# Kernel optimization log

Hardware: AMD Instinct MI355X
Metric: run time of the kernel (lower is better)

Reference implementation:

```python
import jax, jax.numpy as jnp
import numpy as np

NUM_GRAPHS = 128
EPS = 1e-5  # torch BatchNorm1d default eps


def setup_inputs() -> dict:
    key = jax.random.key(0)
    ks = jax.random.split(key, 24)
    N, E, NHE = 50000, 800000, 50000
    NODE_RAW, HEDGE_RAW, H, HH, HOUT = 92, 40, 128, 128, 256
    s = 0.05
    inp = {
        "x": jax.random.normal(ks[0], (N, NODE_RAW), jnp.float32),
        "hedge_attrs": jax.random.normal(ks[1], (NHE, HEDGE_RAW), jnp.float32),
        "inter_relations_index": jax.random.randint(ks[2], (3, E), 0, N, jnp.int64),
        "batch": jax.random.randint(ks[3], (N,), 0, NUM_GRAPHS, jnp.int64),
        "num_nodes": N,
        # embed: Linear(92, h_dim)
        "embed_w": jax.random.normal(ks[4], (NODE_RAW, H), jnp.float32) * s,
        "embed_b": jax.random.normal(ks[5], (H,), jnp.float32) * s,
        # bembed: Linear(hedge_dim, hidden_hedge_dim)
        "bembed_w": jax.random.normal(ks[6], (HEDGE_RAW, HH), jnp.float32) * s,
        "bembed_b": jax.random.normal(ks[7], (HH,), jnp.float32) * s,
        # conv.lin_full_presplit: Linear(2H+HH, 2H)
        "lin_w": jax.random.normal(ks[8], (2 * H + HH, 2 * H), jnp.float32) * s,
        "lin_b": jax.random.normal(ks[9], (2 * H,), jnp.float32) * s,
        "bn1_g": jnp.ones((2 * H,), jnp.float32),
        "bn1_b": jnp.zeros((2 * H,), jnp.float32),
        "bn2_g": jnp.ones((H,), jnp.float32),
        "bn2_b": jnp.zeros((H,), jnp.float32),
        # learnable temperature of SoftmaxAggregation (init 1.0)
        "aggr_t": jnp.ones((), jnp.float32),
        "l1_w": jax.random.normal(ks[10], (H, HOUT), jnp.float32) * s,
        "l1_b": jax.random.normal(ks[11], (HOUT,), jnp.float32) * s,
        "out_w": jax.random.normal(ks[12], (HOUT, 1), jnp.float32) * s,
        "out_b": jax.random.normal(ks[13], (1,), jnp.float32) * s,
    }
    return inp


def _batchnorm(z, g, b):
    mu = z.mean(axis=0)
    var = z.var(axis=0)  # biased, matching torch training-mode normalization
    return (z - mu) * jax.lax.rsqrt(var + EPS) * g + b


def reference(x, hedge_attrs, inter_relations_index, batch, num_nodes,
              embed_w, embed_b, bembed_w, bembed_b, lin_w, lin_b,
              bn1_g, bn1_b, bn2_g, bn2_b, aggr_t, l1_w, l1_b, out_w, out_b):
    idx0 = inter_relations_index[0]
    idx1 = inter_relations_index[1]
    connect_feats = hedge_attrs @ bembed_w + bembed_b          # [NHE, HH]
    h = x @ embed_w + embed_b                                   # [N, H]

    # --- CHGInterConv ---
    origin = h[idx0]                                            # [E, H]
    connect = connect_feats[idx1]                               # [E, HH]
    remote = h[idx0]                                            # faithful to source (uses idx0)
    z = jnp.concatenate([origin, connect, remote], axis=1)      # [E, 2H+HH]
    z = z @ lin_w + lin_b                                       # [E, 2H]
    z = _batchnorm(z, bn1_g, bn1_b)
    z_f, z_c = jnp.split(z, 2, axis=-1)
    msg = jax.nn.sigmoid(z_f) * jax.nn.softplus(z_c)            # [E, H]

    # learned SoftmaxAggregation: per-node, per-channel segment softmax of t*msg
    alpha = msg * aggr_t
    m = jax.ops.segment_max(alpha, idx0, num_segments=num_nodes)
    m = jnp.where(jnp.isfinite(m), m, 0.0)                      # empty segments
    e = jnp.exp(alpha - m[idx0])
    denom = jax.ops.segment_sum(e, idx0, num_segments=num_nodes)
    w = e / (denom[idx0] + 1e-16)
    out = jax.ops.segment_sum(msg * w, idx0, num_segments=num_nodes)  # [N, H]

    out = _batchnorm(out, bn2_g, bn2_b)
    h = jax.nn.softplus(out + h)                                # residual + softplus

    # --- global mean pool over graphs ---
    counts = jax.ops.segment_sum(jnp.ones((num_nodes,), h.dtype), batch,
                                 num_segments=NUM_GRAPHS)
    pooled = jax.ops.segment_sum(h, batch, num_segments=NUM_GRAPHS)
    pooled = pooled / jnp.maximum(counts, 1.0)[:, None]         # [G, H]

    g = jax.nn.softplus(pooled @ l1_w + l1_b)                   # [G, HOUT]
    return g @ out_w + out_b                                    # [G, 1]
```

## Files before the change

### kernel.cpp

```cpp
#include <hip/hip_runtime.h>
#include <hip/hip_bf16.h>


#define EPS_BN 1e-5f
#define LOG2E 1.4426950408889634f
#define LN2   0.6931471805599453f

#define BIN_SH 8
#define BIN_CHUNK 4096

typedef __attribute__((ext_vector_type(8))) short bf16x8;
typedef __attribute__((ext_vector_type(4))) float f32x4;
typedef __attribute__((ext_vector_type(2))) float f32x2;

__device__ __forceinline__ float fexp2(float x) {
#if __has_builtin(__builtin_amdgcn_exp2f)
    return __builtin_amdgcn_exp2f(x);
#else
    return __expf(x * LN2);
#endif
}
__device__ __forceinline__ float flog2(float x) {
#if __has_builtin(__builtin_amdgcn_logf)
    return __builtin_amdgcn_logf(x);
#else
    return __logf(x) * LOG2E;
#endif
}
__device__ __forceinline__ float softplus_fast(float x) {
    return LN2 * flog2(1.f + fexp2(x * LOG2E));
}

__device__ __forceinline__ f32x2 pk_fma2(f32x2 a, f32x2 b, f32x2 c) {
#if __has_builtin(__builtin_elementwise_fma)
    return __builtin_elementwise_fma(a, b, c);
#else
    return (f32x2){fmaf(a.x, b.x, c.x), fmaf(a.y, b.y, c.y)};
#endif
}

__device__ __forceinline__ unsigned short f2bf(float f) {
    unsigned u = __float_as_uint(f);
    unsigned r = (u + 0x7fffu + ((u >> 16) & 1u)) >> 16;
    return (unsigned short)r;
}
__device__ __forceinline__ float bflo(unsigned u) { return __uint_as_float(u << 16); }
__device__ __forceinline__ float bfhi(unsigned u) { return __uint_as_float(u & 0xffff0000u); }
__device__ __forceinline__ float bfu16(unsigned short v) { return __uint_as_float(((unsigned)v) << 16); }
__device__ __forceinline__ unsigned pack2bf(float x, float y) {
    return (unsigned)f2bf(x) | ((unsigned)f2bf(y) << 16);
}

#if __has_builtin(__builtin_amdgcn_cvt_pk_f32_fp8) && __has_builtin(__builtin_amdgcn_cvt_pk_fp8_f32)
#define HW_FP8 1
#else
#define HW_FP8 0
#endif

__device__ __forceinline__ unsigned char f2fp8(float f) {
#if HW_FP8
    int r = __builtin_amdgcn_cvt_pk_fp8_f32(f, f, 0, false);
    return (unsigned char)(r & 0xff);
#else
    unsigned u = __float_as_uint(f);
    unsigned s = (u >> 24) & 0x80u;
    float af = fabsf(f);
    if (!(af >= 0.015625f)) {
        int m = (int)rintf(af * 512.f);
        if (m > 7) m = 7;
        return (unsigned char)(s | (unsigned)m);
    }
    if (af > 448.f) return (unsigned char)(s | 0x7e);
    unsigned au = __float_as_uint(af);
    unsigned r = au + 0x7ffffu + ((au >> 20) & 1u);
    int e8 = (int)(r >> 23) - 120;
    unsigned m = (r >> 20) & 7u;
    if (e8 > 15 || (e8 == 15 && m == 7)) return (unsigned char)(s | 0x7e);
    return (unsigned char)(s | ((unsigned)e8 << 3) | m);
#endif
}

__device__ __forceinline__ void fp8pair(unsigned p, f32x2& lo, f32x2& hi) {
#if HW_FP8
    lo = __builtin_amdgcn_cvt_pk_f32_fp8((int)p, false);
    hi = __builtin_amdgcn_cvt_pk_f32_fp8((int)p, true);
#else
    auto dec = [](unsigned byte) -> float {
        unsigned s = (byte & 0x80u) << 24;
        unsigned em = byte & 0x7fu;
        float nrm = __uint_as_float(s | ((em << 20) + 0x3C000000u));
        float sub = __uint_as_float(s | 0x3F800000u) * (float)em * 0.001953125f;
        return (em >= 8) ? nrm : sub;
    };
    lo = (f32x2){dec(p & 0xff), dec((p >> 8) & 0xff)};
    hi = (f32x2){dec((p >> 16) & 0xff), dec(p >> 24)};
#endif
}

__device__ __forceinline__ int perm256(int j) {
    return (j < 128) ? ((j >> 1) * 4 + (j & 1)) : (((j - 128) >> 1) * 4 + 2 + (j & 1));
}

__global__ __launch_bounds__(256) void k_pre(const float* __restrict__ ew, const float* __restrict__ bw,
                                             const float* __restrict__ lw,
                                             unsigned short* __restrict__ embB, unsigned short* __restrict__ bembB,
                                             unsigned short* __restrict__ waB, unsigned short* __restrict__ wcB,
                                             const int* __restrict__ idx0, const int* __restrict__ batch,
                                             int* __restrict__ bsum, int* __restrict__ gcount,
                                             int E, int N, int NB) {
    const int t = threadIdx.x;
    const int bid = blockIdx.x;
    if (bid >= 320) {
        __shared__ int lhist[256];
        __shared__ int lbat[128];
        const int cb = bid - 320;
        lhist[t] = 0;
        if (t < 128) lbat[t] = 0;
        __syncthreads();
        const int e0 = cb * BIN_CHUNK;
        const int ecnt = min(E - e0, BIN_CHUNK);
        for (int i = t; i < ecnt; i += 256)
            atomicAdd(&lhist[idx0[e0 + i] >> BIN_SH], 1);
        const int n0 = cb * BIN_CHUNK;
        const int ncnt = min(N - n0, BIN_CHUNK);
        for (int i = t; i < ncnt; i += 256)
            atomicAdd(&lbat[batch[n0 + i]], 1);
        __syncthreads();
        if (t < NB && lhist[t]) atomicAdd(&bsum[t], lhist[t]);
        if (t < 128 && lbat[t]) atomicAdd(&gcount[t], lbat[t]);
        return;
    }
    int i = bid * 256 + t;
    if (i >= 81920) return;
    unsigned short* dst;
    int f, NKC, CT, mode;
    if (i < 12288)      { dst = embB;  f = i;         NKC = 3; CT = 2; mode = 0; }
    else if (i < 20480) { dst = bembB; f = i - 12288; NKC = 2; CT = 2; mode = 1; }
    else if (i < 53248) { dst = waB;   f = i - 20480; NKC = 4; CT = 4; mode = 2; }
    else                { dst = wcB;   f = i - 53248; NKC = 4; CT = 4; mode = 3; }
    int j = f & 7, l = (f >> 3) & 63;
    int r2 = f >> 9;
    int c = r2 % CT;
    int r3 = r2 / CT;
    int kc = r3 % NKC, w = r3 / NKC;
    int k = kc * 32 + ((l >> 4) & 3) * 8 + j;
    int n = (w * CT + c) * 16 + (l & 15);
    float v;
    if (mode == 0)      v = (k < 92) ? ew[k * 128 + n] : 0.f;
    else if (mode == 1) v = (k < 40) ? bw[k * 128 + n] : 0.f;
    else if (mode == 2) v = lw[k * 256 + n] + lw[(k + 256) * 256 + n];
    else                v = lw[(k + 128) * 256 + n];
    dst[f] = f2bf(v);
}

__global__ __launch_bounds__(256) void k_scan(const int* __restrict__ bsum, int* __restrict__ boff,
                                              const int* __restrict__ gcount, int* __restrict__ gptr,
                                              const int* __restrict__ batch, int* __restrict__ gfill,
                                              int* __restrict__ pos_of, int N, int NB) {
    __shared__ int s[256];
    const int t = threadIdx.x;
    const int bid = blockIdx.x;
    if (bid == 0) {
        int v = (t < NB) ? bsum[t] : 0;
        s[t] = v;
        __syncthreads();
#pragma unroll
        for (int ofs = 1; ofs < 256; ofs <<= 1) {
            int u = (t >= ofs) ? s[t - ofs] : 0;
            __syncthreads();
            s[t] += u;
            __syncthreads();
        }
        if (t < NB) boff[t] = s[t] - v;
        if (t == NB - 1) boff[NB] = s[t];
        __syncthreads();
        int gv = (t < 128) ? gcount[t] : 0;
        s[t] = gv;
        __syncthreads();
#pragma unroll
        for (int ofs = 1; ofs < 128; ofs <<= 1) {
            int u = (t >= ofs && t < 128) ? s[t - ofs] : 0;
            __syncthreads();
            if (t < 128) s[t] += u;
            __syncthreads();
        }
        if (t < 128) gptr[t + 1] = s[t];
        if (t == 0) gptr[0] = 0;
        return;
    }
    __shared__ int lg[128];
    int gv = (t < 128) ? gcount[t] : 0;
    s[t] = gv;
    __syncthreads();
#pragma unroll
    for (int ofs = 1; ofs < 128; ofs <<= 1) {
        int u = (t >= ofs && t < 128) ? s[t - ofs] : 0;
        __syncthreads();
        if (t < 128) s[t] += u;
        __syncthreads();
    }
    if (t < 128) lg[t] = s[t] - gv;
    __syncthreads();
    int i = (bid - 1) * 256 + t;
    if (i < N) {
        int g = batch[i];
        pos_of[i] = lg[g] + atomicAdd(&gfill[g], 1);
    }
}

template<int KIN, int NKC1, int OMODE2>
__device__ __forceinline__ void gemm_body(
    char* smem, int blk,
    const float* __restrict__ in, const unsigned short* __restrict__ B1, const float* __restrict__ bias1,
    const unsigned short* __restrict__ B2, const float* __restrict__ bias2,
    unsigned short* __restrict__ hout, void* __restrict__ out2, int M,
    const int* __restrict__ pos_of)
{
    const int r0 = blk * 32;
    const int t = threadIdx.x;
    const int w = t >> 6;
    const int l = t & 63;
    const int m = l & 15, q = l >> 4;

    unsigned short* als = (unsigned short*)smem;
    unsigned short* hls = als + 32 * NKC1 * 32;

    const int KP = NKC1 * 32;
    for (int i = t; i < 32 * KP; i += 256) {
        int r = i / KP, k = i - r * KP;
        int gr = r0 + r;
        float v = (gr < M && k < KIN) ? in[(size_t)gr * KIN + k] : 0.f;
        int idx = (((r >> 4) * NKC1 + (k >> 5)) * 64 + ((k >> 3) & 3) * 16 + (r & 15)) * 8 + (k & 7);
        als[idx] = f2bf(v);
    }
    bf16x8 b1[NKC1][2];
    const bf16x8* B1f = (const bf16x8*)B1;
#pragma unroll
    for (int kc = 0; kc < NKC1; kc++)
#pragma unroll
        for (int c = 0; c < 2; c++)
            b1[kc][c] = B1f[((w * NKC1 + kc) * 2 + c) * 64 + l];
    __syncthreads();

    f32x4 acc1[2][2];
#pragma unroll
    for (int c = 0; c < 2; c++) { acc1[c][0] = (f32x4){0.f,0.f,0.f,0.f}; acc1[c][1] = (f32x4){0.f,0.f,0.f,0.f}; }
    const bf16x8* af = (const bf16x8*)als;
#pragma unroll
    for (int kc = 0; kc < NKC1; kc++) {
        bf16x8 a0 = af[kc * 64 + l];
        bf16x8 a1 = af[(NKC1 + kc) * 64 + l];
#pragma unroll
        for (int c = 0; c < 2; c++) {
            acc1[c][0] = __builtin_amdgcn_mfma_f32_16x16x32_bf16(a0, b1[kc][c], acc1[c][0], 0, 0, 0);
            acc1[c][1] = __builtin_amdgcn_mfma_f32_16x16x32_bf16(a1, b1[kc][c], acc1[c][1], 0, 0, 0);
        }
    }
#pragma unroll
    for (int c = 0; c < 2; c++) {
        int n1 = (w * 2 + c) * 16 + m;
        float bv = bias1[n1];
#pragma unroll
        for (int hh = 0; hh < 2; hh++) {
#pragma unroll
            for (int r = 0; r < 4; r++) {
                int row = hh * 16 + q * 4 + r;
                float val = acc1[c][hh][r] + bv;
                unsigned short bf = f2bf(val);
                hls[row * 136 + n1] = bf;
                if (OMODE2 == 1 && r0 + row < M)
                    hout[(size_t)pos_of[r0 + row] * 128 + n1] = bf;
            }
        }
    }
    __syncthreads();

    bf16x8 b2[4][4];
    const bf16x8* B2f = (const bf16x8*)B2;
#pragma unroll
    for (int kc = 0; kc < 4; kc++)
#pragma unroll
        for (int c = 0; c < 4; c++)
            b2[kc][c] = B2f[((w * 4 + kc) * 4 + c) * 64 + l];

    f32x4 acc2[4][2];
#pragma unroll
    for (int c = 0; c < 4; c++) { acc2[c][0] = (f32x4){0.f,0.f,0.f,0.f}; acc2[c][1] = (f32x4){0.f,0.f,0.f,0.f}; }
#pragma unroll
    for (int kc = 0; kc < 4; kc++) {
        bf16x8 a0 = *(const bf16x8*)(hls + m * 136 + kc * 32 + q * 8);
        bf16x8 a1 = *(const bf16x8*)(hls + (m + 16) * 136 + kc * 32 + q * 8);
#pragma unroll
        for (int c = 0; c < 4; c++) {
            acc2[c][0] = __builtin_amdgcn_mfma_f32_16x16x32_bf16(a0, b2[kc][c], acc2[c][0], 0, 0, 0);
            acc2[c][1] = __builtin_amdgcn_mfma_f32_16x16x32_bf16(a1, b2[kc][c], acc2[c][1], 0, 0, 0);
        }
    }
#pragma unroll
    for (int c = 0; c < 4; c++) {
        int n = (w * 4 + c) * 16 + m;
        float bv = bias2 ? bias2[n] : 0.f;
        int pj = perm256(n);
#pragma unroll
        for (int hh = 0; hh < 2; hh++) {
#pragma unroll
            for (int r = 0; r < 4; r++) {
                int row = r0 + hh * 16 + q * 4 + r;
                if (row < M) {
                    float val = acc2[c][hh][r] + bv;
                    if (OMODE2 == 1) ((unsigned short*)out2)[(size_t)row * 256 + pj] = f2bf(val);
                    else             ((unsigned char*)out2)[(size_t)row * 256 + pj] = f2fp8(val);
                }
            }
        }
    }
}

__device__ __forceinline__ void binA_body(
    char* smem, int cb,
    const int* __restrict__ idx0, const int* __restrict__ idx1,
    const int* __restrict__ boff, int* __restrict__ bfill,
    int* __restrict__ staging, int E, int NB)
{
    const int t = threadIdx.x;
    int* svals = (int*)smem;
    unsigned char* sbk = (unsigned char*)(smem + 16384);
    int* lhist = (int*)(smem + 20480);
    int* lbase = (int*)(smem + 21504);
    const int e0 = cb * BIN_CHUNK;
    const int cnt = min(E - e0, BIN_CHUNK);
    for (int b = t; b < NB; b += 256) lhist[b] = 0;
    __syncthreads();
    for (int i = t; i < cnt; i += 256) {
        int n = idx0[e0 + i];
        int m = idx1[e0 + i];
        int bk = n >> BIN_SH;
        sbk[i] = (unsigned char)bk;
        svals[i] = (m << BIN_SH) | (n & ((1 << BIN_SH) - 1));
        atomicAdd(&lhist[bk], 1);
    }
    __syncthreads();
    for (int b = t; b < NB; b += 256) {
        int h = lhist[b];
        int base = h ? atomicAdd(&bfill[b], h) : 0;
        lbase[b] = boff[b] + base;
        lhist[b] = 0;
    }
    __syncthreads();
    for (int i = t; i < cnt; i += 256) {
        int bk = sbk[i];
        int r = atomicAdd(&lhist[bk], 1);
        staging[lbase[bk] + r] = svals[i];
    }
}

__global__ __launch_bounds__(256) void k_main(
    const float* __restrict__ x, const unsigned short* __restrict__ embB, const float* __restrict__ embed_b,
    const unsigned short* __restrict__ waB, const float* __restrict__ lin_b,
    unsigned short* __restrict__ h16, uint2* __restrict__ A16, int N, const int* __restrict__ pos_of,
    const float* __restrict__ hedge, const unsigned short* __restrict__ bembB, const float* __restrict__ bembed_b,
    const unsigned short* __restrict__ wcB, unsigned* __restrict__ Cp8, int NHE,
    const int* __restrict__ idx0, const int* __restrict__ idx1,
    const int* __restrict__ boff, int* __restrict__ bfill, int* __restrict__ staging,
    int E, int NB, int mtN, int mtNHE)
{
    __shared__ __align__(16) char smem[22528];
    const int bid = blockIdx.x;
    if (bid < mtN) {
        gemm_body<92, 3, 1>(smem, bid, x, embB, embed_b, waB, lin_b, h16, (void*)A16, N, pos_of);
    } else if (bid < mtN + mtNHE) {
        gemm_body<40, 2, 2>(smem, bid - mtN, hedge, bembB, bembed_b, wcB, nullptr, nullptr, (void*)Cp8, NHE, nullptr);
    } else {
        binA_body(smem, bid - mtN - mtNHE, idx0, idx1, boff, bfill, staging, E, NB);
    }
}

__global__ __launch_bounds__(256) void k_binB(
    const int* __restrict__ boff, const int* __restrict__ staging,
    int* __restrict__ rowptr, int* __restrict__ sidx1, int* __restrict__ slots,
    int E, int N, int per_slot)
{
    __shared__ int lcnt[256];
    __shared__ int noofs[256];
    __shared__ int s[256];
    const int t = threadIdx.x;
    const int b = blockIdx.x;
    const int n0 = b << BIN_SH;
    const int nn = min(N - n0, 256);
    const int s0 = boff[b], s1 = boff[b + 1];
    lcnt[t] = 0;
    __syncthreads();
    for (int i = s0 + t; i < s1; i += 256)
        atomicAdd(&lcnt[staging[i] & 255], 1);
    __syncthreads();
    int v = lcnt[t];
    s[t] = v;
    __syncthreads();
#pragma unroll
    for (int ofs = 1; ofs < 256; ofs <<= 1) {
        int u = (t >= ofs) ? s[t - ofs] : 0;
        __syncthreads();
        s[t] += u;
        __syncthreads();
    }
    noofs[t] = s[t] - v;
    if (t < nn) rowptr[n0 + t] = s0 + s[t] - v;
    lcnt[t] = 0;
    if (b == 0 && t == 0) rowptr[N] = E;
    __syncthreads();
    if (s1 > s0) {
        int sfirst = (s0 + per_slot - 1) / per_slot;
        int slast  = (s1 - 1) / per_slot;
        for (int si = sfirst + t; si <= slast; si += 256) {
            int tgt = si * per_slot - s0;
            int lo = 0, hi = nn;
            while (lo + 1 < hi) {
                int mid = (lo + hi) >> 1;
                if (noofs[mid] <= tgt) lo = mid; else hi = mid;
            }
            slots[si] = n0 + lo;
        }
    }
    for (int i = s0 + t; i < s1; i += 256) {
        int vv = staging[i];
        int nl = vv & 255;
        int r = atomicAdd(&lcnt[nl], 1);
        sidx1[s0 + noofs[nl] + r] = vv & 0xffffff00;
    }
}

__global__ __launch_bounds__(256) void k_stats(const uint2* __restrict__ A16, const unsigned char* __restrict__ Cp8b,
                                               const int* __restrict__ rowptr, const int* __restrict__ sidx1,
                                               const int* __restrict__ slots,
                                               float* __restrict__ gsum, float* __restrict__ gsq,
                                               int E, int N, int per_slot) {
    __shared__ float4 lsm4[256], lsq4[256];
    const int t = threadIdx.x;
    const int l = t & 63;
    const int wid = __builtin_amdgcn_readfirstlane(t >> 6);
    const int slot = blockIdx.x * 4 + wid;
    const unsigned lo4 = (unsigned)(l << 2);
    const long base = (long)slot * per_slot;
    const int e0 = (int)min((long)E, base);
    const int e1 = (int)min((long)E, base + per_slot);
    f32x2 smF = {0.f,0.f}, smC = {0.f,0.f};
    f32x2 sqF = {0.f,0.f}, sqC = {0.f,0.f};
    f32x2 csrF = {0.f,0.f}, csrC = {0.f,0.f};
    f32x2 aF = {0.f,0.f}, aC = {0.f,0.f};
    int cur_n = 0, bound = 0, runk = 0;

    auto flush = [&]() {
        if (runk) {
            float fk = (float)runk;
            f32x2 fk2 = {fk, fk};
            smF += csrF; smC += csrC;
            smF = pk_fma2(fk2, aF, smF);
            smC = pk_fma2(fk2, aC, smC);
            f32x2 tF = pk_fma2(fk2, aF, csrF + csrF);
            f32x2 tC = pk_fma2(fk2, aC, csrC + csrC);
            sqF = pk_fma2(aF, tF, sqF);
            sqC = pk_fma2(aC, tC, sqC);
        }
        csrF = (f32x2){0.f,0.f}; csrC = (f32x2){0.f,0.f};
        runk = 0;
    };
    auto loadA = [&](int n) {
        uint2 a8 = A16[(size_t)n * 64 + l];
        aF = (f32x2){bflo(a8.x), bfhi(a8.x)};
        aC = (f32x2){bflo(a8.y), bfhi(a8.y)};
    };

    if (e0 < e1) {
        cur_n = __builtin_amdgcn_readfirstlane(slots[slot]);
        bound = __builtin_amdgcn_readfirstlane(rowptr[cur_n + 1]);
        loadA(cur_n);
    }

    auto proc = [&](int e, unsigned p) {
        if (e >= bound) {
            flush();
            do { cur_n++; bound = __builtin_amdgcn_readfirstlane(rowptr[cur_n + 1]); } while (bound <= e);
            loadA(cur_n);
        }
        f32x2 vf, vc;
        fp8pair(p, vf, vc);
        csrF += vf; csrC += vc;
        sqF = pk_fma2(vf, vf, sqF);
        sqC = pk_fma2(vc, vc, sqC);
        runk++;
    };

    const int nfull = (e1 - e0) & ~7;
    if (nfull > 0) {
        int eg = e0;
        unsigned cur[8];
        {
            int4 m0 = *(const int4*)(sidx1 + eg);
            int4 m1 = *(const int4*)(sidx1 + eg + 4);
            cur[0] = *(const unsigned*)(Cp8b + ((unsigned)m0.x + lo4));
            cur[1] = *(const unsigned*)(Cp8b + ((unsigned)m0.y + lo4));
            cur[2] = *(const unsigned*)(Cp8b + ((unsigned)m0.z + lo4));
            cur[3] = *(const unsigned*)(Cp8b + ((unsigned)m0.w + lo4));
            cur[4] = *(const unsigned*)(Cp8b + ((unsigned)m1.x + lo4));
            cur[5] = *(const unsigned*)(Cp8b + ((unsigned)m1.y + lo4));
            cur[6] = *(const unsigned*)(Cp8b + ((unsigned)m1.z + lo4));
            cur[7] = *(const unsigned*)(Cp8b + ((unsigned)m1.w + lo4));
        }
        for (;;) {
            const int en = eg + 8;
            const bool more = en < e0 + nfull;
            unsigned nxt[8];
            if (more) {
                int4 t0 = *(const int4*)(sidx1 + en);
                int4 t1 = *(const int4*)(sidx1 + en + 4);
                nxt[0] = *(const unsigned*)(Cp8b + ((unsigned)t0.x + lo4));
                nxt[1] = *(const unsigned*)(Cp8b + ((unsigned)t0.y + lo4));
                nxt[2] = *(const unsigned*)(Cp8b + ((unsigned)t0.z + lo4));
                nxt[3] = *(const unsigned*)(Cp8b + ((unsigned)t0.w + lo4));
                nxt[4] = *(const unsigned*)(Cp8b + ((unsigned)t1.x + lo4));
                nxt[5] = *(const unsigned*)(Cp8b + ((unsigned)t1.y + lo4));
                nxt[6] = *(const unsigned*)(Cp8b + ((unsigned)t1.z + lo4));
                nxt[7] = *(const unsigned*)(Cp8b + ((unsigned)t1.w + lo4));
            }
            proc(eg, cur[0]);     proc(eg + 1, cur[1]);
            proc(eg + 2, cur[2]); proc(eg + 3, cur[3]);
            proc(eg + 4, cur[4]); proc(eg + 5, cur[5]);
            proc(eg + 6, cur[6]); proc(eg + 7, cur[7]);
            if (!more) break;
#pragma unroll
            for (int i = 0; i < 8; i++) cur[i] = nxt[i];
            eg = en;
        }
    }
    for (int e = e0 + nfull; e < e1; e++)
        proc(e, *(const unsigned*)(Cp8b + ((unsigned)sidx1[e] + lo4)));
    flush();

    lsm4[t] = (float4){smF.x, smF.y, smC.x, smC.y};
    lsq4[t] = (float4){sqF.x, sqF.y, sqC.x, sqC.y};
    __syncthreads();
    const float* fm = (const float*)lsm4;
    const float* fq = (const float*)lsq4;
    float vs = fm[t] + fm[256 + t] + fm[512 + t] + fm[768 + t];
    float vq = fq[t] + fq[256 + t] + fq[512 + t] + fq[768 + t];
    atomicAdd(&gsum[t], vs);
    atomicAdd(&gsq[t], vq);
}

__global__ __launch_bounds__(256) void k_aggr(const uint2* __restrict__ A16, const unsigned char* __restrict__ Cp8b,
                                              const int* __restrict__ rowptr, const int* __restrict__ sidx1,
                                              const int* __restrict__ pos_of,
                                              const float* __restrict__ bn1_sum, const float* __restrict__ bn1_sq,
                                              const float* __restrict__ g1, const float* __restrict__ b1,
                                              const float* __restrict__ tptr, unsigned* __restrict__ out,
                                              float invE, int N) {
    const int t = threadIdx.x;
    const int l = t & 63;
    const int wid = __builtin_amdgcn_readfirstlane(t >> 6);
    const int n = blockIdx.x * 4 + wid;
    if (n >= N) return;

    const int e0 = __builtin_amdgcn_readfirstlane(rowptr[n]);
    const int e1 = __builtin_amdgcn_readfirstlane(rowptr[n + 1]);
    const int pn = __builtin_amdgcn_readfirstlane(pos_of[n]);

    const float tt = tptr[0];
    const float4 sum4 = ((const float4*)bn1_sum)[l];
    const float4 sq4  = ((const float4*)bn1_sq)[l];
    const float2 gf = ((const float2*)g1)[l];
    const float2 gc = ((const float2*)(g1 + 128))[l];
    const float2 bf2 = ((const float2*)b1)[l];
    const float2 bc2 = ((const float2*)(b1 + 128))[l];
    auto mkss = [&](float sum, float sq, float gg, float bb, float& sc, float& sh) {
        float mu = sum * invE;
        float var = sq * invE - mu * mu;
        sc = gg * rsqrtf(var + EPS_BN);
        sh = fmaf(-mu, sc, bb);
    };
    float scx, shx, scy, shy, scz, shz, scw, shw;
    mkss(sum4.x, sq4.x, gf.x, bf2.x, scx, shx);
    mkss(sum4.y, sq4.y, gf.y, bf2.y, scy, shy);
    mkss(sum4.z, sq4.z, gc.x, bc2.x, scz, shz);
    mkss(sum4.w, sq4.w, gc.y, bc2.y, scw, shw);
    const f32x2 sF  = {-scx * LOG2E, -scy * LOG2E};
    const f32x2 sC  = { scz * LOG2E,  scw * LOG2E};

    uint2 a8 = A16[(size_t)n * 64 + l];
    f32x2 aF = {bflo(a8.x), bfhi(a8.x)}, aC = {bflo(a8.y), bfhi(a8.y)};
    const f32x2 bF = pk_fma2(aF, sF, (f32x2){-shx * LOG2E, -shy * LOG2E});
    const f32x2 bC = pk_fma2(aC, sC, (f32x2){ shz * LOG2E,  shw * LOG2E});

    if (e0 >= e1) { out[(size_t)pn * 64 + l] = 0u; return; }

    const unsigned lo4 = (unsigned)(l << 2);
    f32x2 den = {0.f,0.f}, num = {0.f,0.f};

    auto G = [&](int e) -> unsigned {
        return *(const unsigned*)(Cp8b + ((unsigned)sidx1[e] + lo4));
    };
    auto procg = [&](unsigned p) {
        f32x2 vf, vc;
        fp8pair(p, vf, vc);
        f32x2 argf = pk_fma2(vf, sF, bF);
        f32x2 argc = pk_fma2(vc, sC, bC);
        f32x2 ef = {fexp2(argf.x), fexp2(argf.y)};
        f32x2 uu = {fexp2(argc.x), fexp2(argc.y)};
        f32x2 d1 = ef + 1.f;
        f32x2 u1 = uu + 1.f;
        f32x2 sig = {__builtin_amdgcn_rcpf(d1.x), __builtin_amdgcn_rcpf(d1.y)};
        f32x2 lg = {flog2(u1.x), flog2(u1.y)};
        f32x2 M = sig * lg;
        f32x2 tM = M * tt;
        f32x2 w = {fexp2(tM.x), fexp2(tM.y)};
        den += w;
        num = pk_fma2(M, w, num);
    };

    const int cnt = e1 - e0;
    unsigned cur[8];
#pragma unroll
    for (int i = 0; i < 8; i++)
        if (i < cnt) cur[i] = G(e0 + i);

    int e = e0;
    while (e + 8 < e1) {
        unsigned nxt[8];
#pragma unroll
        for (int i = 0; i < 8; i++)
            if (e + 8 + i < e1) nxt[i] = G(e + 8 + i);
#pragma unroll
        for (int i = 0; i < 8; i++) procg(cur[i]);
#pragma unroll
        for (int i = 0; i < 8; i++) cur[i] = nxt[i];
        e += 8;
    }
    const int rem = e1 - e;
#pragma unroll
    for (int i = 0; i < 8; i++)
        if (i < rem) procg(cur[i]);

    float ox = LN2 * num.x * __builtin_amdgcn_rcpf(den.x);
    float oy = LN2 * num.y * __builtin_amdgcn_rcpf(den.y);
    out[(size_t)pn * 64 + l] = pack2bf(ox, oy);
}

__global__ __launch_bounds__(256) void k_bn2stats(const unsigned* __restrict__ outw, float* __restrict__ sum,
                                                  float* __restrict__ sq, int N) {
    __shared__ float4 ls[256];
    const int t = threadIdx.x;
    const int w = t & 63;
    const int rg = t >> 6;
    f32x2 sm = {0.f,0.f}, s2 = {0.f,0.f};
    for (int n = blockIdx.x * 4 + rg; n < N; n += gridDim.x * 4) {
        unsigned v = outw[(size_t)n * 64 + w];
        f32x2 x = {bflo(v), bfhi(v)};
        sm += x;
        s2 = pk_fma2(x, x, s2);
    }
    ls[t] = (float4){sm.x, sm.y, s2.x, s2.y};
    __syncthreads();
    if (t < 64) {
        float4 a = ls[t], b = ls[t + 64], c = ls[t + 128], d = ls[t + 192];
        atomicAdd(&sum[2 * w],     a.x + b.x + c.x + d.x);
        atomicAdd(&sum[2 * w + 1], a.y + b.y + c.y + d.y);
        atomicAdd(&sq[2 * w],      a.z + b.z + c.z + d.z);
        atomicAdd(&sq[2 * w + 1],  a.w + b.w + c.w + d.w);
    }
}

template<int SPLIT>
__global__ __launch_bounds__(128) void k_h2pool(const unsigned short* __restrict__ out,
                                                const unsigned short* __restrict__ h,
                                                const int* __restrict__ gptr,
                                                const float* __restrict__ bn2_sum, const float* __restrict__ bn2_sq,
                                                const float* __restrict__ g2, const float* __restrict__ b2,
                                                float* __restrict__ pooled, float invN) {
    const int g = blockIdx.x & 127;
    const int sp = blockIdx.x >> 7;
    const int c = threadIdx.x;
    float mu = bn2_sum[c] * invN;
    float var = bn2_sq[c] * invN - mu * mu;
    float sc = g2[c] * rsqrtf(var + EPS_BN);
    float sh = fmaf(-mu, sc, b2[c]);
    const int i0 = gptr[g], i1 = gptr[g + 1];
    float acc = 0.f;
    for (int i = i0 + sp; i < i1; i += SPLIT) {
        float v = fmaf(bfu16(out[(size_t)i * 128 + c]), sc, sh) + bfu16(h[(size_t)i * 128 + c]);
        acc += softplus_fast(v);
    }
    if (acc != 0.f) atomicAdd(&pooled[g * 128 + c], acc);
}

__global__ __launch_bounds__(256) void k_head(const float* __restrict__ pooled, const int* __restrict__ gcount,
                                              const float* __restrict__ l1w, const float* __restrict__ l1b,
                                              const float* __restrict__ outw, const float* __restrict__ outb,
                                              float* __restrict__ dout) {
    __shared__ float p[128];
    __shared__ float red[256];
    const int g = blockIdx.x;
    const int j = threadIdx.x;
    if (j < 128) {
        float cnt = (float)max(gcount[g], 1);
        p[j] = pooled[g * 128 + j] / cnt;
    }
    __syncthreads();
    float acc = l1b[j];
    for (int k = 0; k < 128; k++) acc = fmaf(p[k], l1w[k * 256 + j], acc);
    red[j] = softplus_fast(acc) * outw[j];
    __syncthreads();
    for (int s = 128; s > 0; s >>= 1) {
        if (j < s) red[j] += red[j + s];
        __syncthreads();
    }
    if (j == 0) dout[g] = red[0] + outb[0];
}

extern "C" void kernel_launch(void* const* d_in, const int* in_sizes, int n_in,
                              void* d_out, int out_size, void* d_ws, size_t ws_size,
                              hipStream_t stream) {
    const float* x        = (const float*)d_in[0];
    const float* hedge    = (const float*)d_in[1];
    const int*   iri      = (const int*)d_in[2];
    const int*   batch    = (const int*)d_in[3];
    const float* embed_w  = (const float*)d_in[5];
    const float* embed_b  = (const float*)d_in[6];
    const float* bembed_w = (const float*)d_in[7];
    const float* bembed_b = (const float*)d_in[8];
    const float* lin_w    = (const float*)d_in[9];
    const float* lin_b    = (const float*)d_in[10];
    const float* bn1_g    = (const float*)d_in[11];
    const float* bn1_b    = (const float*)d_in[12];
    const float* bn2_g    = (const float*)d_in[13];
    const float* bn2_b    = (const float*)d_in[14];
    const float* aggr_t   = (const float*)d_in[15];
    const float* l1_w     = (const float*)d_in[16];
    const float* l1_b     = (const float*)d_in[17];
    const float* out_w    = (const float*)d_in[18];
    const float* out_b    = (const float*)d_in[19];

    const int N   = in_sizes[0] / 92;
    const int NHE = in_sizes[1] / 40;
    const int E   = in_sizes[2] / 3;
    const int* idx0 = iri;
    const int* idx1 = iri + E;

    float* ws = (float*)d_ws;
    size_t off = 0;
    auto alloc = [&](size_t elems) -> float* {
        float* p = ws + off;
        off += (elems + 63) & ~(size_t)63;
        return p;
    };
    unsigned short* h16 = (unsigned short*)alloc((size_t)N * 64);
    uint2* A16    = (uint2*)alloc((size_t)N * 128);
    unsigned* Cp8 = (unsigned*)alloc((size_t)NHE * 64);
    unsigned short* embB  = (unsigned short*)alloc(6144);
    unsigned short* bembB = (unsigned short*)alloc(4096);
    unsigned short* waB   = (unsigned short*)alloc(16384);
    unsigned short* wcB   = (unsigned short*)alloc(16384);
    int*   rowptr = (int*)alloc((size_t)N + 1);
    int*   boff   = (int*)alloc(260);
    int*   sidx1  = (int*)alloc((size_t)E + 8);
    int*   staging = (int*)alloc((size_t)E + 8);
    int*   gptr   = (int*)alloc(129);
    int*   pos_of = (int*)alloc((size_t)N);
    int*   slots  = (int*)alloc(8200);
    unsigned* outbuf = (unsigned*)alloc((size_t)N * 64);
    float* zbase  = ws + off;
    int*   bsum   = (int*)alloc(256);
    int*   bfill  = (int*)alloc(256);
    int*   gfill  = (int*)alloc(128);
    int*   gcount = (int*)alloc(128);
    float* bn1_sum = alloc(256);
    float* bn1_sq  = alloc(256);
    float* bn2_sum = alloc(128);
    float* bn2_sq  = alloc(128);
    float* pooled  = alloc(128 * 128);
    size_t zbytes = (size_t)((ws + off) - zbase) * sizeof(float);
    (void)ws_size;

    hipMemsetAsync(zbase, 0, zbytes, stream);

    const int NB = (N + 255) >> BIN_SH;
    const int EB = (E + BIN_CHUNK - 1) / BIN_CHUNK;
    const int GB = (N + 255) / 256;

    k_pre<<<320 + EB, 256, 0, stream>>>(embed_w, bembed_w, lin_w, embB, bembB, waB, wcB,
                                        idx0, batch, bsum, gcount, E, N, NB);

    k_scan<<<1 + GB, 256, 0, stream>>>(bsum, boff, gcount, gptr, batch, gfill, pos_of, N, NB);

    const int mtN   = (N + 31) / 32;
    const int mtNHE = (NHE + 31) / 32;
    k_main<<<mtN + mtNHE + EB, 256, 0, stream>>>(
        x, embB, embed_b, waB, lin_b, h16, A16, N, pos_of,
        hedge, bembB, bembed_b, wcB, Cp8, NHE,
        idx0, idx1, boff, bfill, staging, E, NB, mtN, mtNHE);

    const int EDGE_BLOCKS = 2048;
    const int NSLOTS = EDGE_BLOCKS * 4;
    int per_slot = ((E + NSLOTS - 1) / NSLOTS + 7) & ~7;
    k_binB<<<NB, 256, 0, stream>>>(boff, staging, rowptr, sidx1, slots, E, N, per_slot);

    k_stats<<<EDGE_BLOCKS, 256, 0, stream>>>(A16, (const unsigned char*)Cp8, rowptr, sidx1, slots,
                                             bn1_sum, bn1_sq, E, N, per_slot);

    k_aggr<<<(N + 3) / 4, 256, 0, stream>>>(A16, (const unsigned char*)Cp8, rowptr, sidx1, pos_of,
                                            bn1_sum, bn1_sq, bn1_g, bn1_b, aggr_t, outbuf,
                                            1.0f / (float)E, N);

    k_bn2stats<<<256, 256, 0, stream>>>((const unsigned*)outbuf, bn2_sum, bn2_sq, N);
    k_h2pool<16><<<128 * 16, 128, 0, stream>>>((const unsigned short*)outbuf, h16, gptr,
                                               bn2_sum, bn2_sq, bn2_g, bn2_b, pooled, 1.0f / (float)N);

    k_head<<<128, 256, 0, stream>>>(pooled, gcount, l1_w, l1_b, out_w, out_b, (float*)d_out);
}
```

Baseline: 386.0 us.

## Fuse front and tail kernels into cooperative launches with grid syncs

Merges the memset, weight-pack/histogram, and scan kernels into one cooperative kernel separated by grid.sync, and merges the BN2 stats, pooling, and head kernels into a second cooperative kernel. The aim is to cut kernel launch overheads and inter-kernel gaps on a short pipeline. The cost is grid-wide barriers and a requirement that every block be co-resident. The tail also changes its split, using 1024 blocks of 256 threads in place of 2048 blocks of 128, and skips atomics that would add zero.

```diff
diff --git a/kernel.cpp b/kernel.cpp
--- a/kernel.cpp
+++ b/kernel.cpp
@@ -1,5 +1,8 @@
 #include <hip/hip_runtime.h>
 #include <hip/hip_bf16.h>
+#include <hip/hip_cooperative_groups.h>
+
+namespace cg = cooperative_groups;
 
 
 #define EPS_BN 1e-5f
@@ -101,18 +104,30 @@
     return (j < 128) ? ((j >> 1) * 4 + (j & 1)) : (((j - 128) >> 1) * 4 + 2 + (j & 1));
 }
 
-__global__ __launch_bounds__(256) void k_pre(const float* __restrict__ ew, const float* __restrict__ bw,
-                                             const float* __restrict__ lw,
-                                             unsigned short* __restrict__ embB, unsigned short* __restrict__ bembB,
-                                             unsigned short* __restrict__ waB, unsigned short* __restrict__ wcB,
-                                             const int* __restrict__ idx0, const int* __restrict__ batch,
-                                             int* __restrict__ bsum, int* __restrict__ gcount,
-                                             int E, int N, int NB) {
+__global__ __launch_bounds__(256) void k_front(
+    const float* __restrict__ ew, const float* __restrict__ bw, const float* __restrict__ lw,
+    unsigned short* __restrict__ embB, unsigned short* __restrict__ bembB,
+    unsigned short* __restrict__ waB, unsigned short* __restrict__ wcB,
+    const int* __restrict__ idx0, const int* __restrict__ batch,
+    int* __restrict__ bsum, int* __restrict__ gcount,
+    float* __restrict__ zbase, int zwords,
+    int* __restrict__ boff, int* __restrict__ gptr, int* __restrict__ gfill,
+    int* __restrict__ pos_of,
+    int E, int N, int NB, int EB, int GB)
+{
+    cg::grid_group grid = cg::this_grid();
+    __shared__ int s[256];
+    __shared__ int lg[128];
+    __shared__ int lhist[256];
+    __shared__ int lbat[128];
     const int t = threadIdx.x;
     const int bid = blockIdx.x;
-    if (bid >= 320) {
-        __shared__ int lhist[256];
-        __shared__ int lbat[128];
+
+    for (int i = bid * 256 + t; i < zwords; i += gridDim.x * 256)
+        ((int*)zbase)[i] = 0;
+    grid.sync();
+
+    if (bid >= 320 && bid < 320 + EB) {
         const int cb = bid - 320;
         lhist[t] = 0;
         if (t < 128) lbat[t] = 0;
@@ -128,38 +143,32 @@
         __syncthreads();
         if (t < NB && lhist[t]) atomicAdd(&bsum[t], lhist[t]);
         if (t < 128 && lbat[t]) atomicAdd(&gcount[t], lbat[t]);
-        return;
-    }
-    int i = bid * 256 + t;
-    if (i >= 81920) return;
-    unsigned short* dst;
-    int f, NKC, CT, mode;
-    if (i < 12288)      { dst = embB;  f = i;         NKC = 3; CT = 2; mode = 0; }
-    else if (i < 20480) { dst = bembB; f = i - 12288; NKC = 2; CT = 2; mode = 1; }
-    else if (i < 53248) { dst = waB;   f = i - 20480; NKC = 4; CT = 4; mode = 2; }
-    else                { dst = wcB;   f = i - 53248; NKC = 4; CT = 4; mode = 3; }
-    int j = f & 7, l = (f >> 3) & 63;
-    int r2 = f >> 9;
-    int c = r2 % CT;
-    int r3 = r2 / CT;
-    int kc = r3 % NKC, w = r3 / NKC;
-    int k = kc * 32 + ((l >> 4) & 3) * 8 + j;
-    int n = (w * CT + c) * 16 + (l & 15);
-    float v;
-    if (mode == 0)      v = (k < 92) ? ew[k * 128 + n] : 0.f;
-    else if (mode == 1) v = (k < 40) ? bw[k * 128 + n] : 0.f;
-    else if (mode == 2) v = lw[k * 256 + n] + lw[(k + 256) * 256 + n];
-    else                v = lw[(k + 128) * 256 + n];
-    dst[f] = f2bf(v);
-}
-
-__global__ __launch_bounds__(256) void k_scan(const int* __restrict__ bsum, int* __restrict__ boff,
-                                              const int* __restrict__ gcount, int* __restrict__ gptr,
-                                              const int* __restrict__ batch, int* __restrict__ gfill,
-                                              int* __restrict__ pos_of, int N, int NB) {
-    __shared__ int s[256];
-    const int t = threadIdx.x;
-    const int bid = blockIdx.x;
+    } else if (bid < 320) {
+        int i = bid * 256 + t;
+        if (i < 81920) {
+            unsigned short* dst;
+            int f, NKC, CT, mode;
+            if (i < 12288)      { dst = embB;  f = i;         NKC = 3; CT = 2; mode = 0; }
+            else if (i < 20480) { dst = bembB; f = i - 12288; NKC = 2; CT = 2; mode = 1; }
+            else if (i < 53248) { dst = waB;   f = i - 20480; NKC = 4; CT = 4; mode = 2; }
+            else                { dst = wcB;   f = i - 53248; NKC = 4; CT = 4; mode = 3; }
+            int j = f & 7, l = (f >> 3) & 63;
+            int r2 = f >> 9;
+            int c = r2 % CT;
+            int r3 = r2 / CT;
+            int kc = r3 % NKC, w = r3 / NKC;
+            int k = kc * 32 + ((l >> 4) & 3) * 8 + j;
+            int n = (w * CT + c) * 16 + (l & 15);
+            float v;
+            if (mode == 0)      v = (k < 92) ? ew[k * 128 + n] : 0.f;
+            else if (mode == 1) v = (k < 40) ? bw[k * 128 + n] : 0.f;
+            else if (mode == 2) v = lw[k * 256 + n] + lw[(k + 256) * 256 + n];
+            else                v = lw[(k + 128) * 256 + n];
+            dst[f] = f2bf(v);
+        }
+    }
+    grid.sync();
+
     if (bid == 0) {
         int v = (t < NB) ? bsum[t] : 0;
         s[t] = v;
@@ -186,25 +195,24 @@
         }
         if (t < 128) gptr[t + 1] = s[t];
         if (t == 0) gptr[0] = 0;
-        return;
-    }
-    __shared__ int lg[128];
-    int gv = (t < 128) ? gcount[t] : 0;
-    s[t] = gv;
-    __syncthreads();
-#pragma unroll
-    for (int ofs = 1; ofs < 128; ofs <<= 1) {
-        int u = (t >= ofs && t < 128) ? s[t - ofs] : 0;
-        __syncthreads();
-        if (t < 128) s[t] += u;
-        __syncthreads();
-    }
-    if (t < 128) lg[t] = s[t] - gv;
-    __syncthreads();
-    int i = (bid - 1) * 256 + t;
-    if (i < N) {
-        int g = batch[i];
-        pos_of[i] = lg[g] + atomicAdd(&gfill[g], 1);
+    } else if (bid <= GB) {
+        int gv = (t < 128) ? gcount[t] : 0;
+        s[t] = gv;
+        __syncthreads();
+#pragma unroll
+        for (int ofs = 1; ofs < 128; ofs <<= 1) {
+            int u = (t >= ofs && t < 128) ? s[t - ofs] : 0;
+            __syncthreads();
+            if (t < 128) s[t] += u;
+            __syncthreads();
+        }
+        if (t < 128) lg[t] = s[t] - gv;
+        __syncthreads();
+        int i = (bid - 1) * 256 + t;
+        if (i < N) {
+            int g = batch[i];
+            pos_of[i] = lg[g] + atomicAdd(&gfill[g], 1);
+        }
     }
 }
 
@@ -644,75 +652,86 @@
     out[(size_t)pn * 64 + l] = pack2bf(ox, oy);
 }
 
-__global__ __launch_bounds__(256) void k_bn2stats(const unsigned* __restrict__ outw, float* __restrict__ sum,
-                                                  float* __restrict__ sq, int N) {
-    __shared__ float4 ls[256];
+__global__ __launch_bounds__(256) void k_tail(
+    const unsigned* __restrict__ outw, const unsigned short* __restrict__ h16,
+    const int* __restrict__ gptr,
+    float* __restrict__ bn2_sum, float* __restrict__ bn2_sq,
+    const float* __restrict__ g2, const float* __restrict__ b2,
+    float* __restrict__ pooled, const int* __restrict__ gcount,
+    const float* __restrict__ l1w, const float* __restrict__ l1b,
+    const float* __restrict__ outw_h, const float* __restrict__ outb,
+    float* __restrict__ dout, int N, float invN)
+{
+    cg::grid_group grid = cg::this_grid();
     const int t = threadIdx.x;
-    const int w = t & 63;
-    const int rg = t >> 6;
-    f32x2 sm = {0.f,0.f}, s2 = {0.f,0.f};
-    for (int n = blockIdx.x * 4 + rg; n < N; n += gridDim.x * 4) {
-        unsigned v = outw[(size_t)n * 64 + w];
-        f32x2 x = {bflo(v), bfhi(v)};
-        sm += x;
-        s2 = pk_fma2(x, x, s2);
-    }
-    ls[t] = (float4){sm.x, sm.y, s2.x, s2.y};
-    __syncthreads();
-    if (t < 64) {
-        float4 a = ls[t], b = ls[t + 64], c = ls[t + 128], d = ls[t + 192];
-        atomicAdd(&sum[2 * w],     a.x + b.x + c.x + d.x);
-        atomicAdd(&sum[2 * w + 1], a.y + b.y + c.y + d.y);
-        atomicAdd(&sq[2 * w],      a.z + b.z + c.z + d.z);
-        atomicAdd(&sq[2 * w + 1],  a.w + b.w + c.w + d.w);
-    }
-}
-
-template<int SPLIT>
-__global__ __launch_bounds__(128) void k_h2pool(const unsigned short* __restrict__ out,
-                                                const unsigned short* __restrict__ h,
-                                                const int* __restrict__ gptr,
-                                                const float* __restrict__ bn2_sum, const float* __restrict__ bn2_sq,
-                                                const float* __restrict__ g2, const float* __restrict__ b2,
-                                                float* __restrict__ pooled, float invN) {
-    const int g = blockIdx.x & 127;
-    const int sp = blockIdx.x >> 7;
-    const int c = threadIdx.x;
-    float mu = bn2_sum[c] * invN;
-    float var = bn2_sq[c] * invN - mu * mu;
-    float sc = g2[c] * rsqrtf(var + EPS_BN);
-    float sh = fmaf(-mu, sc, b2[c]);
-    const int i0 = gptr[g], i1 = gptr[g + 1];
-    float acc = 0.f;
-    for (int i = i0 + sp; i < i1; i += SPLIT) {
-        float v = fmaf(bfu16(out[(size_t)i * 128 + c]), sc, sh) + bfu16(h[(size_t)i * 128 + c]);
-        acc += softplus_fast(v);
-    }
-    if (acc != 0.f) atomicAdd(&pooled[g * 128 + c], acc);
-}
-
-__global__ __launch_bounds__(256) void k_head(const float* __restrict__ pooled, const int* __restrict__ gcount,
-                                              const float* __restrict__ l1w, const float* __restrict__ l1b,
-                                              const float* __restrict__ outw, const float* __restrict__ outb,
-                                              float* __restrict__ dout) {
-    __shared__ float p[128];
-    __shared__ float red[256];
-    const int g = blockIdx.x;
-    const int j = threadIdx.x;
-    if (j < 128) {
-        float cnt = (float)max(gcount[g], 1);
-        p[j] = pooled[g * 128 + j] / cnt;
-    }
-    __syncthreads();
-    float acc = l1b[j];
-    for (int k = 0; k < 128; k++) acc = fmaf(p[k], l1w[k * 256 + j], acc);
-    red[j] = softplus_fast(acc) * outw[j];
-    __syncthreads();
-    for (int s = 128; s > 0; s >>= 1) {
-        if (j < s) red[j] += red[j + s];
-        __syncthreads();
-    }
-    if (j == 0) dout[g] = red[0] + outb[0];
+    const int bid = blockIdx.x;
+
+    {
+        __shared__ float4 ls[256];
+        const int w = t & 63;
+        const int rg = t >> 6;
+        f32x2 sm = {0.f,0.f}, s2 = {0.f,0.f};
+        for (int n = bid * 4 + rg; n < N; n += gridDim.x * 4) {
+            unsigned v = outw[(size_t)n * 64 + w];
+            f32x2 x = {bflo(v), bfhi(v)};
+            sm += x;
+            s2 = pk_fma2(x, x, s2);
+        }
+        ls[t] = (float4){sm.x, sm.y, s2.x, s2.y};
+        __syncthreads();
+        if (t < 64) {
+            float4 a = ls[t], b = ls[t + 64], c = ls[t + 128], d = ls[t + 192];
+            float vx = a.x + b.x + c.x + d.x;
+            float vy = a.y + b.y + c.y + d.y;
+            float vz = a.z + b.z + c.z + d.z;
+            float vw = a.w + b.w + c.w + d.w;
+            if (vx != 0.f) atomicAdd(&bn2_sum[2 * t], vx);
+            if (vy != 0.f) atomicAdd(&bn2_sum[2 * t + 1], vy);
+            if (vz != 0.f) atomicAdd(&bn2_sq[2 * t], vz);
+            if (vw != 0.f) atomicAdd(&bn2_sq[2 * t + 1], vw);
+        }
+    }
+    grid.sync();
+
+    {
+        const unsigned short* out16 = (const unsigned short*)outw;
+        const int g = bid & 127;
+        const int sp = ((bid >> 7) << 1) + (t >> 7);
+        const int c = t & 127;
+        float mu = bn2_sum[c] * invN;
+        float var = bn2_sq[c] * invN - mu * mu;
+        float sc = g2[c] * rsqrtf(var + EPS_BN);
+        float sh = fmaf(-mu, sc, b2[c]);
+        const int i0 = gptr[g], i1 = gptr[g + 1];
+        float acc = 0.f;
+        for (int i = i0 + sp; i < i1; i += 16) {
+            float v = fmaf(bfu16(out16[(size_t)i * 128 + c]), sc, sh) + bfu16(h16[(size_t)i * 128 + c]);
+            acc += softplus_fast(v);
+        }
+        if (acc != 0.f) atomicAdd(&pooled[g * 128 + c], acc);
+    }
+    grid.sync();
+
+    if (bid < 128) {
+        __shared__ float p[128];
+        __shared__ float red[256];
+        const int g = bid;
+        const int j = t;
+        if (j < 128) {
+            float cnt = (float)max(gcount[g], 1);
+            p[j] = pooled[g * 128 + j] / cnt;
+        }
+        __syncthreads();
+        float acc = l1b[j];
+        for (int k = 0; k < 128; k++) acc = fmaf(p[k], l1w[k * 256 + j], acc);
+        red[j] = softplus_fast(acc) * outw_h[j];
+        __syncthreads();
+        for (int s = 128; s > 0; s >>= 1) {
+            if (j < s) red[j] += red[j + s];
+            __syncthreads();
+        }
+        if (j == 0) dout[g] = red[0] + outb[0];
+    }
 }
 
 extern "C" void kernel_launch(void* const* d_in, const int* in_sizes, int n_in,
@@ -776,19 +795,26 @@
     float* bn2_sum = alloc(128);
     float* bn2_sq  = alloc(128);
     float* pooled  = alloc(128 * 128);
-    size_t zbytes = (size_t)((ws + off) - zbase) * sizeof(float);
+    int zwords = (int)((ws + off) - zbase);
     (void)ws_size;
-
-    hipMemsetAsync(zbase, 0, zbytes, stream);
 
     const int NB = (N + 255) >> BIN_SH;
     const int EB = (E + BIN_CHUNK - 1) / BIN_CHUNK;
     const int GB = (N + 255) / 256;
 
-    k_pre<<<320 + EB, 256, 0, stream>>>(embed_w, bembed_w, lin_w, embB, bembB, waB, wcB,
-                                        idx0, batch, bsum, gcount, E, N, NB);
-
-    k_scan<<<1 + GB, 256, 0, stream>>>(bsum, boff, gcount, gptr, batch, gfill, pos_of, N, NB);
+    {
+        int FG = 320 + EB;
+        void* args[] = {
+            (void*)&embed_w, (void*)&bembed_w, (void*)&lin_w,
+            (void*)&embB, (void*)&bembB, (void*)&waB, (void*)&wcB,
+            (void*)&idx0, (void*)&batch,
+            (void*)&bsum, (void*)&gcount,
+            (void*)&zbase, (void*)&zwords,
+            (void*)&boff, (void*)&gptr, (void*)&gfill, (void*)&pos_of,
+            (void*)&E, (void*)&N, (void*)&NB, (void*)&EB, (void*)&GB
+        };
+        hipLaunchCooperativeKernel((const void*)k_front, dim3(FG), dim3(256), args, 0, stream);
+    }
 
     const int mtN   = (N + 31) / 32;
     const int mtNHE = (NHE + 31) / 32;
@@ -809,9 +835,17 @@
                                             bn1_sum, bn1_sq, bn1_g, bn1_b, aggr_t, outbuf,
                                             1.0f / (float)E, N);
 
-    k_bn2stats<<<256, 256, 0, stream>>>((const unsigned*)outbuf, bn2_sum, bn2_sq, N);
-    k_h2pool<16><<<128 * 16, 128, 0, stream>>>((const unsigned short*)outbuf, h16, gptr,
-                                               bn2_sum, bn2_sq, bn2_g, bn2_b, pooled, 1.0f / (float)N);
-
-    k_head<<<128, 256, 0, stream>>>(pooled, gcount, l1_w, l1_b, out_w, out_b, (float*)d_out);
-}
+    {
+        float invN = 1.0f / (float)N;
+        const unsigned* outw = outbuf;
+        void* args[] = {
+            (void*)&outw, (void*)&h16, (void*)&gptr,
+            (void*)&bn2_sum, (void*)&bn2_sq,
+            (void*)&bn2_g, (void*)&bn2_b,
+            (void*)&pooled, (void*)&gcount,
+            (void*)&l1_w, (void*)&l1_b, (void*)&out_w, (void*)&out_b,
+            (void*)&d_out, (void*)&N, (void*)&invN
+        };
+        hipLaunchCooperativeKernel((const void*)k_tail, dim3(1024), dim3(256), args, 0, stream);
+    }
+}
```

New measurement: 686.0 us. 77.7% more time.
